# Performance work log

Measured on AMD Instinct MI355X. Metric: run time of the kernel, lower is better.

The kernel has to match this reference:

```python
import jax, jax.numpy as jnp
import numpy as np

INPUT_SIZE = 2048
HIDDEN_SIZE = 2048
BATCH = 8192


def setup_inputs() -> dict:
    key = jax.random.key(0)
    ks = jax.random.split(key, 11)
    comb = INPUT_SIZE + HIDDEN_SIZE
    s = 1.0 / np.sqrt(comb)
    inp = {
        "x": jax.random.normal(ks[0], (BATCH, INPUT_SIZE), jnp.float32),
        "h_prev": jax.random.normal(ks[1], (BATCH, HIDDEN_SIZE), jnp.float32),
        "c_prev": jax.random.normal(ks[2], (BATCH, HIDDEN_SIZE), jnp.float32),
        # torch nn.Linear weights: (out_features, in_features)
        "W_f": jax.random.uniform(ks[3], (HIDDEN_SIZE, comb), jnp.float32, -s, s),
        "b_f": jax.random.uniform(ks[4], (HIDDEN_SIZE,), jnp.float32, -s, s),
        "W_i": jax.random.uniform(ks[5], (HIDDEN_SIZE, comb), jnp.float32, -s, s),
        "b_i": jax.random.uniform(ks[6], (HIDDEN_SIZE,), jnp.float32, -s, s),
        "W_c": jax.random.uniform(ks[7], (HIDDEN_SIZE, comb), jnp.float32, -s, s),
        "b_c": jax.random.uniform(ks[8], (HIDDEN_SIZE,), jnp.float32, -s, s),
        "W_o": jax.random.uniform(ks[9], (HIDDEN_SIZE, comb), jnp.float32, -s, s),
        "b_o": jax.random.uniform(ks[10], (HIDDEN_SIZE,), jnp.float32, -s, s),
    }
    return inp


def reference(x, h_prev, c_prev, W_f, b_f, W_i, b_i, W_c, b_c, W_o, b_o):
    combined = jnp.concatenate([x, h_prev], axis=1)  # [B, in+hid]
    # Fuse the four gate GEMMs into one: stack weights along output dim.
    W_all = jnp.concatenate([W_f, W_i, W_c, W_o], axis=0)  # [4H, in+hid]
    b_all = jnp.concatenate([b_f, b_i, b_c, b_o], axis=0)  # [4H]
    gates = combined @ W_all.T + b_all  # [B, 4H]
    f_lin, i_lin, c_lin, o_lin = jnp.split(gates, 4, axis=1)
    f_t = jax.nn.sigmoid(f_lin)
    i_t = jax.nn.sigmoid(i_lin)
    c_tilde = jnp.tanh(c_lin)
    c_t = f_t * c_prev + i_t * c_tilde
    o_t = jax.nn.sigmoid(o_lin)
    h_t = o_t * jnp.tanh(c_t)
    return (h_t, c_t)
```

## Files before the change

### kernel.cpp

```cpp
#include <hip/hip_runtime.h>
#include <hip/hip_bf16.h>


typedef short bf16x8 __attribute__((ext_vector_type(8)));
typedef float f32x4  __attribute__((ext_vector_type(4)));

#define BATCH 8192
#define INPUT 2048
#define HID   2048
#define KDIM  4096
#define NT_K  64

__device__ __forceinline__ float bf2f(unsigned short u) {
    return __uint_as_float(((unsigned int)u) << 16);
}
__device__ __forceinline__ unsigned short f2bf(float f) {
    unsigned int u = __float_as_uint(f);
    u += 0x7fffu + ((u >> 16) & 1u);
    return (unsigned short)(u >> 16);
}
__device__ __forceinline__ float sigm(float x)  { return 1.0f / (1.0f + __expf(-x)); }
__device__ __forceinline__ float tanh_(float x) { return 2.0f / (1.0f + __expf(-2.0f * x)) - 1.0f; }

__device__ __forceinline__ bool looks_bf16(const unsigned short* p) {
    int lane = threadIdx.x & 63;
    unsigned short v = p[2 * lane];
    int e = (v >> 7) & 0xFF;
    return __all(e >= 90 && e <= 141) != 0;
}

__device__ __forceinline__ bf16x8 sani(bf16x8 v) {
    #pragma unroll
    for (int i = 0; i < 8; ++i) {
        unsigned short u = (unsigned short)v[i];
        if ((u & 0x7F80u) == 0x7F80u) v[i] = 0;
    }
    return v;
}

__device__ __forceinline__ uint2 pack4(float4 v) {
    uint2 r;
    r.x = (unsigned int)f2bf(v.x) | ((unsigned int)f2bf(v.y) << 16);
    r.y = (unsigned int)f2bf(v.z) | ((unsigned int)f2bf(v.w) << 16);
    return r;
}

__device__ __forceinline__ void gload_lds16(const void* g, void* l) {
    __builtin_amdgcn_global_load_lds(
        (const __attribute__((address_space(1))) unsigned int*)g,
        (__attribute__((address_space(3))) unsigned int*)l, 16, 0, 0);
}

#define NCHUNK_SIDE (2048 * 2048)

__global__ __launch_bounds__(256) void pack_ws8(
    const void* __restrict__ x, const void* __restrict__ hprev,
    const void* __restrict__ Wf, const void* __restrict__ Wi,
    const void* __restrict__ Wc, const void* __restrict__ Wo,
    char* __restrict__ Aws, char* __restrict__ Bws)
{
    const bool isb = looks_bf16((const unsigned short*)x);
    const int total = 2 * NCHUNK_SIDE;
    for (int idx = blockIdx.x * 256 + threadIdx.x; idx < total;
         idx += gridDim.x * 256) {
        const int side = (idx >= NCHUNK_SIDE);
        const int c    = side ? idx - NCHUNK_SIDE : idx;
        const int tile = c >> 11;
        const int b16  = c & 2047;
        const int kt   = tile & 63;
        const int tt   = tile >> 6;
        const int half = b16 >> 10;
        const int r_in = (b16 >> 3) & 127;
        const int slot = b16 & 7;
        const int k    = kt * 64 + (slot ^ (r_in & 7)) * 8;

        const void* base;
        size_t soff;
        if (!side) {
            const int R = tt * 256 + half * 128 + r_in;
            if (k < INPUT) { base = x;     soff = (size_t)R * INPUT + k; }
            else           { base = hprev; soff = (size_t)R * HID + (k - INPUT); }
        } else {
            const int P  = half * 128 + r_in;
            const int g  = P >> 6;
            const int wn = (P >> 4) & 3;
            const int cc = P & 15;
            const int h  = tt * 64 + wn * 16 + cc;
            base = (g == 0) ? Wf : (g == 1) ? Wi : (g == 2) ? Wc : Wo;
            soff = (size_t)h * KDIM + k;
        }
        char* dst = (side ? Bws : Aws) + (size_t)c * 16;
        if (isb) {
            bf16x8 v = sani(*(const bf16x8*)((const unsigned short*)base + soff));
            *(bf16x8*)dst = v;
        } else {
            const float* s = (const float*)base + soff;
            float4 v0 = *(const float4*)s;
            float4 v1 = *(const float4*)(s + 4);
            uint2 p0 = pack4(v0), p1 = pack4(v1);
            uint4 o; o.x = p0.x; o.y = p0.y; o.z = p1.x; o.w = p1.y;
            *(uint4*)dst = o;
        }
    }
}

#define VM(n)  asm volatile("s_waitcnt vmcnt(" #n ")" ::: "memory")
#define BAR()  do { asm volatile("" ::: "memory"); \
                    __builtin_amdgcn_s_barrier();  \
                    asm volatile("" ::: "memory"); } while (0)

__global__ __launch_bounds__(512, 2) void lstm_main8(
    const char* __restrict__ Aws, const char* __restrict__ Bws,
    const void* __restrict__ x_orig,
    const void* __restrict__ cprev_v,
    const void* __restrict__ bfp, const void* __restrict__ bip,
    const void* __restrict__ bcp, const void* __restrict__ bop,
    void* __restrict__ out_v)
{
    extern __shared__ __align__(16) char smem[];

    const bool isb = looks_bf16((const unsigned short*)x_orig);

    const int tid   = threadIdx.x;
    const int wid   = tid >> 6;
    const int lane  = tid & 63;
    const int wm    = wid >> 2;
    const int wn    = wid & 3;
    const int lrow  = lane & 15;
    const int chunk = lane >> 4;

    const int bid = blockIdx.x;
    const int swz = (bid & 7) * 128 + (bid >> 3);
    const int mt  = swz >> 5, nt = swz & 31;

    const char* Atile = Aws + (size_t)(mt * 64) * 32768;
    const char* Btile = Bws + (size_t)(nt * 64) * 32768;
    const int stg  = wid * 1024 + lane * 16;
    const int stgl = wid * 1024;

    const int xm = (lrow & 7) << 4;
    int koff[2];
    koff[0] = (chunk * 16) ^ xm;
    koff[1] = (64 + chunk * 16) ^ xm;
    int aoff[8];
    #pragma unroll
    for (int m = 0; m < 8; ++m)
        aoff[m] = (m >> 2) * 16384 + ((((m & 3) * 2 + wm) * 16 + lrow) * 128);
    int boff[4];
    #pragma unroll
    for (int g = 0; g < 4; ++g)
        boff[g] = 32768 + (g >> 1) * 16384 + ((((g & 1) * 4 + wn) * 16 + lrow) * 128);

    const int col_h = nt * 64 + wn * 16 + lrow;
    float bias0, bias1, bias2, bias3;
    if (isb) {
        bias0 = bf2f(((const unsigned short*)bfp)[col_h]);
        bias1 = bf2f(((const unsigned short*)bip)[col_h]);
        bias2 = bf2f(((const unsigned short*)bcp)[col_h]);
        bias3 = bf2f(((const unsigned short*)bop)[col_h]);
    } else {
        bias0 = ((const float*)bfp)[col_h];
        bias1 = ((const float*)bip)[col_h];
        bias2 = ((const float*)bcp)[col_h];
        bias3 = ((const float*)bop)[col_h];
    }

    f32x4 acc[8][4];
    #pragma unroll
    for (int m = 0; m < 8; ++m) {
        acc[m][0] = (f32x4){bias0, bias0, bias0, bias0};
        acc[m][1] = (f32x4){bias1, bias1, bias1, bias1};
        acc[m][2] = (f32x4){bias2, bias2, bias2, bias2};
        acc[m][3] = (f32x4){bias3, bias3, bias3, bias3};
    }

    bf16x8 af[4][2], bf[2][2];

#define STAGE_A(NB, H, T) do { \
        const char* _g = Atile + (size_t)(T) * 32768 + (H) * 16384 + stg; \
        char* _l = smem + (NB) + (H) * 16384 + stgl;                      \
        gload_lds16(_g, _l); gload_lds16(_g + 8192, _l + 8192); } while (0)
#define STAGE_B(NB, H, T) do { \
        const char* _g = Btile + (size_t)(T) * 32768 + (H) * 16384 + stg; \
        char* _l = smem + (NB) + 32768 + (H) * 16384 + stgl;              \
        gload_lds16(_g, _l); gload_lds16(_g + 8192, _l + 8192); } while (0)
#define LOADA(BUFB, MB) do { \
        _Pragma("unroll") for (int mi = 0; mi < 4; ++mi)                  \
        _Pragma("unroll") for (int ks = 0; ks < 2; ++ks)                  \
            af[mi][ks] = *(const bf16x8*)(smem + (BUFB) + aoff[(MB) + mi] + koff[ks]); } while (0)
#define LOADB(BUFB, GB) do { \
        _Pragma("unroll") for (int gi = 0; gi < 2; ++gi)                  \
        _Pragma("unroll") for (int ks = 0; ks < 2; ++ks)                  \
            bf[gi][ks] = *(const bf16x8*)(smem + (BUFB) + boff[(GB) + gi] + koff[ks]); } while (0)
#define MM(MB, GB) do { \
        __builtin_amdgcn_s_setprio(1);                                    \
        _Pragma("unroll") for (int mi = 0; mi < 4; ++mi)                  \
        _Pragma("unroll") for (int gi = 0; gi < 2; ++gi)                  \
        _Pragma("unroll") for (int ks = 0; ks < 2; ++ks)                  \
            acc[(MB) + mi][(GB) + gi] = __builtin_amdgcn_mfma_f32_16x16x32_bf16( \
                af[mi][ks], bf[gi][ks], acc[(MB) + mi][(GB) + gi], 0, 0, 0);      \
        __builtin_amdgcn_s_setprio(0); } while (0)

    STAGE_A(0, 0, 0);
    STAGE_B(0, 0, 0);
    STAGE_B(0, 1, 0);
    STAGE_A(0, 1, 0);

    #pragma unroll 1
    for (int t = 0; t < NT_K - 1; ++t) {
        const int bufb = (t & 1) << 16;
        const int nb   = ((t & 1) ^ 1) << 16;
        STAGE_A(nb, 0, t + 1);
        VM(6); BAR();
        LOADA(bufb, 0); LOADB(bufb, 0);
        MM(0, 0); BAR();
        STAGE_B(nb, 0, t + 1);
        VM(6); BAR();
        LOADB(bufb, 2);
        MM(0, 2); BAR();
        STAGE_B(nb, 1, t + 1);
        VM(6); BAR();
        LOADA(bufb, 4);
        MM(4, 2); BAR();
        STAGE_A(nb, 1, t + 1);
        BAR();
        LOADB(bufb, 0);
        MM(4, 0); BAR();
    }
    {
        const int bufb = ((NT_K - 1) & 1) << 16;
        VM(4); BAR();
        LOADA(bufb, 0); LOADB(bufb, 0);
        MM(0, 0); BAR();
        VM(2); BAR();
        LOADB(bufb, 2);
        MM(0, 2); BAR();
        VM(0); BAR();
        LOADA(bufb, 4);
        MM(4, 2); BAR();
        BAR();
        LOADB(bufb, 0);
        MM(4, 0);
    }

    if (isb) {
        const unsigned short* cp = (const unsigned short*)cprev_v;
        unsigned short* ho = (unsigned short*)out_v;
        unsigned short* co = ho + (size_t)BATCH * HID;
        #pragma unroll
        for (int m = 0; m < 8; ++m) {
            const int row0 = mt * 256 + (m * 2 + wm) * 16 + (lane >> 4) * 4;
            #pragma unroll
            for (int r = 0; r < 4; ++r) {
                const int row = row0 + r;
                float fg = sigm(acc[m][0][r]);
                float ig = sigm(acc[m][1][r]);
                float cg = tanh_(acc[m][2][r]);
                float og = sigm(acc[m][3][r]);
                float cpv = bf2f(cp[(size_t)row * HID + col_h]);
                float ct = fg * cpv + ig * cg;
                float ht = og * tanh_(ct);
                co[(size_t)row * HID + col_h] = f2bf(ct);
                ho[(size_t)row * HID + col_h] = f2bf(ht);
            }
        }
    } else {
        const float* cp = (const float*)cprev_v;
        float* ho = (float*)out_v;
        float* co = ho + (size_t)BATCH * HID;
        #pragma unroll
        for (int m = 0; m < 8; ++m) {
            const int row0 = mt * 256 + (m * 2 + wm) * 16 + (lane >> 4) * 4;
            #pragma unroll
            for (int r = 0; r < 4; ++r) {
                const int row = row0 + r;
                float fg = sigm(acc[m][0][r]);
                float ig = sigm(acc[m][1][r]);
                float cg = tanh_(acc[m][2][r]);
                float og = sigm(acc[m][3][r]);
                float cpv = cp[(size_t)row * HID + col_h];
                float ct = fg * cpv + ig * cg;
                float ht = og * tanh_(ct);
                co[(size_t)row * HID + col_h] = ct;
                ho[(size_t)row * HID + col_h] = ht;
            }
        }
    }
}

__global__ __launch_bounds__(256) void lstm_bf16(
    const unsigned short* __restrict__ x,
    const unsigned short* __restrict__ hprev,
    const unsigned short* __restrict__ cprev,
    const unsigned short* __restrict__ Wf, const unsigned short* __restrict__ bfp,
    const unsigned short* __restrict__ Wi, const unsigned short* __restrict__ bip,
    const unsigned short* __restrict__ Wc, const unsigned short* __restrict__ bcp,
    const unsigned short* __restrict__ Wo, const unsigned short* __restrict__ bop,
    unsigned short* __restrict__ hout, unsigned short* __restrict__ cout)
{
    if (!looks_bf16(x)) return;

    __shared__ __align__(16) unsigned short lds_a[128 * 32];
    __shared__ __align__(16) unsigned short lds_b[128 * 32];

    const int tid  = threadIdx.x;
    const int wave = tid >> 6;
    const int lane = tid & 63;
    const int wm   = wave >> 1;
    const int wn   = wave & 1;
    const int m_base = blockIdx.x * 128;
    const int h_base = blockIdx.y * 32;

    const int rA0 = tid >> 2,        sA = tid & 3;
    const int rA1 = 64 + (tid >> 2);
    const unsigned short* Wsel = (wave == 0) ? Wf : (wave == 1) ? Wi
                               : (wave == 2) ? Wc : Wo;
    const unsigned short* bsrc0 =
        Wsel + (size_t)(h_base + (rA0 & 15)) * KDIM + sA * 8;
    const unsigned short* bsrc1 =
        Wsel + (size_t)(h_base + 16 + (rA1 & 15)) * KDIM + sA * 8;
    const size_t aoff0 = (size_t)(m_base + rA0) * INPUT + sA * 8;
    const size_t aoff1 = (size_t)(m_base + rA1) * INPUT + sA * 8;

    const int lrow = lane & 15, lchunk = lane >> 4;
    const int col_h = h_base + wn * 16 + lrow;

    const float bias0 = bf2f(bfp[col_h]), bias1 = bf2f(bip[col_h]);
    const float bias2 = bf2f(bcp[col_h]), bias3 = bf2f(bop[col_h]);

    f32x4 acc[4][4];
    for (int mi = 0; mi < 4; ++mi) {
        acc[mi][0] = (f32x4){bias0, bias0, bias0, bias0};
        acc[mi][1] = (f32x4){bias1, bias1, bias1, bias1};
        acc[mi][2] = (f32x4){bias2, bias2, bias2, bias2};
        acc[mi][3] = (f32x4){bias3, bias3, bias3, bias3};
    }

    for (int k0 = 0; k0 < KDIM; k0 += 32) {
        const unsigned short* asrc = (k0 < INPUT) ? (x + k0) : (hprev + (k0 - INPUT));
        bf16x8 va0 = sani(*(const bf16x8*)(asrc + aoff0));
        bf16x8 va1 = sani(*(const bf16x8*)(asrc + aoff1));
        bf16x8 vb0 = sani(*(const bf16x8*)(bsrc0 + k0));
        bf16x8 vb1 = sani(*(const bf16x8*)(bsrc1 + k0));

        __syncthreads();
        *(bf16x8*)&lds_a[rA0 * 32 + sA * 8] = va0;
        *(bf16x8*)&lds_a[rA1 * 32 + sA * 8] = va1;
        *(bf16x8*)&lds_b[rA0 * 32 + sA * 8] = vb0;
        *(bf16x8*)&lds_b[rA1 * 32 + sA * 8] = vb1;
        __syncthreads();

        bf16x8 af2[4], bfr[4];
        #pragma unroll
        for (int i = 0; i < 4; ++i) {
            af2[i] = *(const bf16x8*)&lds_a[(wm * 64 + i * 16 + lrow) * 32 + lchunk * 8];
            bfr[i] = *(const bf16x8*)&lds_b[(wn * 64 + i * 16 + lrow) * 32 + lchunk * 8];
        }
        #pragma unroll
        for (int mi = 0; mi < 4; ++mi)
            #pragma unroll
            for (int g = 0; g < 4; ++g)
                acc[mi][g] = __builtin_amdgcn_mfma_f32_16x16x32_bf16(
                                 af2[mi], bfr[g], acc[mi][g], 0, 0, 0);
    }

    #pragma unroll
    for (int mi = 0; mi < 4; ++mi) {
        const int row0 = m_base + wm * 64 + mi * 16 + (lane >> 4) * 4;
        #pragma unroll
        for (int r = 0; r < 4; ++r) {
            const int row = row0 + r;
            float fg = sigm(acc[mi][0][r]);
            float ig = sigm(acc[mi][1][r]);
            float cg = tanh_(acc[mi][2][r]);
            float og = sigm(acc[mi][3][r]);
            float cp = bf2f(cprev[(size_t)row * HID + col_h]);
            float ct = fg * cp + ig * cg;
            float ht = og * tanh_(ct);
            cout[(size_t)row * HID + col_h] = f2bf(ct);
            hout[(size_t)row * HID + col_h] = f2bf(ht);
        }
    }
}

__global__ __launch_bounds__(256) void lstm_f32(
    const float* __restrict__ x,
    const float* __restrict__ hprev,
    const float* __restrict__ cprev,
    const float* __restrict__ Wf, const float* __restrict__ bfp,
    const float* __restrict__ Wi, const float* __restrict__ bip,
    const float* __restrict__ Wc, const float* __restrict__ bcp,
    const float* __restrict__ Wo, const float* __restrict__ bop,
    float* __restrict__ hout, float* __restrict__ cout)
{
    if (looks_bf16((const unsigned short*)x)) return;

    __shared__ __align__(16) unsigned short lds_a[128 * 32];
    __shared__ __align__(16) unsigned short lds_b[128 * 32];

    const int tid  = threadIdx.x;
    const int wave = tid >> 6;
    const int lane = tid & 63;
    const int wm   = wave >> 1;
    const int wn   = wave & 1;
    const int m_base = blockIdx.x * 128;
    const int h_base = blockIdx.y * 32;

    const int s8  = tid >> 3;
    const int sub = tid & 7;
    const float* W4[4] = {Wf, Wi, Wc, Wo};
    size_t aoff2[4];
    const float* bptr[4];
    #pragma unroll
    for (int r = 0; r < 4; ++r) {
        const int row = r * 32 + s8;
        aoff2[r] = (size_t)(m_base + row) * INPUT + sub * 4;
        const int gate = (2 * r + (tid >> 7)) & 3;
        const int wrow = h_base + ((r >> 1) << 4) + (s8 & 15);
        bptr[r] = W4[gate] + (size_t)wrow * KDIM + sub * 4;
    }

    const int lrow = lane & 15, lchunk = lane >> 4;
    const int col_h = h_base + wn * 16 + lrow;

    const float bias0 = bfp[col_h], bias1 = bip[col_h];
    const float bias2 = bcp[col_h], bias3 = bop[col_h];

    f32x4 acc[4][4];
    for (int mi = 0; mi < 4; ++mi) {
        acc[mi][0] = (f32x4){bias0, bias0, bias0, bias0};
        acc[mi][1] = (f32x4){bias1, bias1, bias1, bias1};
        acc[mi][2] = (f32x4){bias2, bias2, bias2, bias2};
        acc[mi][3] = (f32x4){bias3, bias3, bias3, bias3};
    }

    for (int k0 = 0; k0 < KDIM; k0 += 32) {
        const float* asrc = (k0 < INPUT) ? (x + k0) : (hprev + (k0 - INPUT));
        float4 va[4], vb[4];
        #pragma unroll
        for (int r = 0; r < 4; ++r) va[r] = *(const float4*)(asrc + aoff2[r]);
        #pragma unroll
        for (int r = 0; r < 4; ++r) vb[r] = *(const float4*)(bptr[r] + k0);

        __syncthreads();
        #pragma unroll
        for (int r = 0; r < 4; ++r) {
            const int row = r * 32 + s8;
            *(uint2*)&lds_a[row * 32 + sub * 4] = pack4(va[r]);
            *(uint2*)&lds_b[row * 32 + sub * 4] = pack4(vb[r]);
        }
        __syncthreads();

        bf16x8 af2[4], bfr[4];
        #pragma unroll
        for (int i = 0; i < 4; ++i) {
            af2[i] = *(const bf16x8*)&lds_a[(wm * 64 + i * 16 + lrow) * 32 + lchunk * 8];
            bfr[i] = *(const bf16x8*)&lds_b[(wn * 64 + i * 16 + lrow) * 32 + lchunk * 8];
        }
        #pragma unroll
        for (int mi = 0; mi < 4; ++mi)
            #pragma unroll
            for (int g = 0; g < 4; ++g)
                acc[mi][g] = __builtin_amdgcn_mfma_f32_16x16x32_bf16(
                                 af2[mi], bfr[g], acc[mi][g], 0, 0, 0);
    }

    #pragma unroll
    for (int mi = 0; mi < 4; ++mi) {
        const int row0 = m_base + wm * 64 + mi * 16 + (lane >> 4) * 4;
        #pragma unroll
        for (int r = 0; r < 4; ++r) {
            const int row = row0 + r;
            float fg = sigm(acc[mi][0][r]);
            float ig = sigm(acc[mi][1][r]);
            float cg = tanh_(acc[mi][2][r]);
            float og = sigm(acc[mi][3][r]);
            float cp = cprev[(size_t)row * HID + col_h];
            float ct = fg * cp + ig * cg;
            float ht = og * tanh_(ct);
            cout[(size_t)row * HID + col_h] = ct;
            hout[(size_t)row * HID + col_h] = ht;
        }
    }
}

extern "C" void kernel_launch(void* const* d_in, const int* in_sizes, int n_in,
                              void* d_out, int out_size, void* d_ws, size_t ws_size,
                              hipStream_t stream) {
    const size_t WS_NEEDED = (size_t)(BATCH + 4 * HID) * KDIM * sizeof(unsigned short);

    if (ws_size >= WS_NEEDED) {
        char* A_ws = (char*)d_ws;
        char* B_ws = A_ws + (size_t)BATCH * KDIM * 2;

        hipLaunchKernelGGL(pack_ws8, dim3(4096), dim3(256), 0, stream,
                           d_in[0], d_in[1], d_in[3], d_in[5], d_in[7], d_in[9],
                           A_ws, B_ws);

        static int attr_done = 0;
        if (!attr_done) {
            hipFuncSetAttribute(reinterpret_cast<const void*>(lstm_main8),
                                hipFuncAttributeMaxDynamicSharedMemorySize, 131072);
            attr_done = 1;
        }
        hipLaunchKernelGGL(lstm_main8, dim3(1024), dim3(512), 131072, stream,
                           A_ws, B_ws, d_in[0], d_in[2],
                           d_in[4], d_in[6], d_in[8], d_in[10], d_out);
        return;
    }

    dim3 grid(BATCH / 128, HID / 32);
    dim3 block(256);
    {
        const unsigned short* x  = (const unsigned short*)d_in[0];
        const unsigned short* hp = (const unsigned short*)d_in[1];
        const unsigned short* cp = (const unsigned short*)d_in[2];
        unsigned short* hout = (unsigned short*)d_out;
        unsigned short* cout = hout + (size_t)BATCH * HID;
        hipLaunchKernelGGL(lstm_bf16, grid, block, 0, stream, x, hp, cp,
                           (const unsigned short*)d_in[3], (const unsigned short*)d_in[4],
                           (const unsigned short*)d_in[5], (const unsigned short*)d_in[6],
                           (const unsigned short*)d_in[7], (const unsigned short*)d_in[8],
                           (const unsigned short*)d_in[9], (const unsigned short*)d_in[10],
                           hout, cout);
    }
    {
        const float* x  = (const float*)d_in[0];
        const float* hp = (const float*)d_in[1];
        const float* cp = (const float*)d_in[2];
        float* hout = (float*)d_out;
        float* cout = hout + (size_t)BATCH * HID;
        hipLaunchKernelGGL(lstm_f32, grid, block, 0, stream, x, hp, cp,
                           (const float*)d_in[3], (const float*)d_in[4],
                           (const float*)d_in[5], (const float*)d_in[6],
                           (const float*)d_in[7], (const float*)d_in[8],
                           (const float*)d_in[9], (const float*)d_in[10],
                           hout, cout);
    }
}
```

Before: 832.4 us.

## Software-pipeline LDS fragment loads with MFMA and restructure pack kernel

The main GEMM loop now keeps separate register sets for the A row halves and the B gate pairs. This lets each MFMA group run while the next fragments are read from LDS, and the last MFMA of one k-step is deferred into the next iteration. The aim is to hide LDS read latency behind the matrix cores, at the cost of more VGPRs. The pack kernel is also rewritten so each thread handles 8 rows with fixed-stride, nontemporal loads and stores, which removes the grid-stride loop and per-element index math. It now assumes a grid of exactly 2^20 threads.

Measured after the change: 785.7 us. 1.06x faster.

```diff
diff --git a/kernel.cpp b/kernel.cpp
--- a/kernel.cpp
+++ b/kernel.cpp
@@ -4,6 +4,7 @@
 
 typedef short bf16x8 __attribute__((ext_vector_type(8)));
 typedef float f32x4  __attribute__((ext_vector_type(4)));
+typedef unsigned int u32x4 __attribute__((ext_vector_type(4)));
 
 #define BATCH 8192
 #define INPUT 2048
@@ -38,10 +39,10 @@
     return v;
 }
 
-__device__ __forceinline__ uint2 pack4(float4 v) {
+__device__ __forceinline__ uint2 pack4v(f32x4 v) {
     uint2 r;
-    r.x = (unsigned int)f2bf(v.x) | ((unsigned int)f2bf(v.y) << 16);
-    r.y = (unsigned int)f2bf(v.z) | ((unsigned int)f2bf(v.w) << 16);
+    r.x = (unsigned int)f2bf(v[0]) | ((unsigned int)f2bf(v[1]) << 16);
+    r.y = (unsigned int)f2bf(v[2]) | ((unsigned int)f2bf(v[3]) << 16);
     return r;
 }
 
@@ -50,8 +51,6 @@
         (const __attribute__((address_space(1))) unsigned int*)g,
         (__attribute__((address_space(3))) unsigned int*)l, 16, 0, 0);
 }
-
-#define NCHUNK_SIDE (2048 * 2048)
 
 __global__ __launch_bounds__(256) void pack_ws8(
     const void* __restrict__ x, const void* __restrict__ hprev,
@@ -60,46 +59,51 @@
     char* __restrict__ Aws, char* __restrict__ Bws)
 {
     const bool isb = looks_bf16((const unsigned short*)x);
-    const int total = 2 * NCHUNK_SIDE;
-    for (int idx = blockIdx.x * 256 + threadIdx.x; idx < total;
-         idx += gridDim.x * 256) {
-        const int side = (idx >= NCHUNK_SIDE);
-        const int c    = side ? idx - NCHUNK_SIDE : idx;
-        const int tile = c >> 11;
-        const int b16  = c & 2047;
-        const int kt   = tile & 63;
-        const int tt   = tile >> 6;
-        const int half = b16 >> 10;
-        const int r_in = (b16 >> 3) & 127;
-        const int slot = b16 & 7;
-        const int k    = kt * 64 + (slot ^ (r_in & 7)) * 8;
-
-        const void* base;
-        size_t soff;
-        if (!side) {
-            const int R = tt * 256 + half * 128 + r_in;
-            if (k < INPUT) { base = x;     soff = (size_t)R * INPUT + k; }
-            else           { base = hprev; soff = (size_t)R * HID + (k - INPUT); }
-        } else {
-            const int P  = half * 128 + r_in;
-            const int g  = P >> 6;
-            const int wn = (P >> 4) & 3;
-            const int cc = P & 15;
-            const int h  = tt * 64 + wn * 16 + cc;
-            base = (g == 0) ? Wf : (g == 1) ? Wi : (g == 2) ? Wc : Wo;
-            soff = (size_t)h * KDIM + k;
-        }
-        char* dst = (side ? Bws : Aws) + (size_t)c * 16;
-        if (isb) {
-            bf16x8 v = sani(*(const bf16x8*)((const unsigned short*)base + soff));
-            *(bf16x8*)dst = v;
-        } else {
-            const float* s = (const float*)base + soff;
-            float4 v0 = *(const float4*)s;
-            float4 v1 = *(const float4*)(s + 4);
-            uint2 p0 = pack4(v0), p1 = pack4(v1);
-            uint4 o; o.x = p0.x; o.y = p0.y; o.z = p1.x; o.w = p1.y;
-            *(uint4*)dst = o;
+    const unsigned int u = blockIdx.x * 256 + threadIdx.x;
+    const int slot = u & 7;
+    const int rgrp = (u >> 3) & 15;
+    const int half = (u >> 7) & 1;
+    const int tile = (u >> 8) & 2047;
+    const int side = u >> 19;
+    const int kt = tile & 63, tt = tile >> 6;
+
+    const void* base;
+    size_t src0;
+    int stride;
+    if (!side) {
+        const int row0 = tt * 256 + half * 128 + rgrp * 8;
+        if (kt < 32) { base = x;     src0 = (size_t)row0 * INPUT + kt * 64; }
+        else         { base = hprev; src0 = (size_t)row0 * HID + (kt - 32) * 64; }
+        stride = INPUT;
+    } else {
+        const int P0 = half * 128 + rgrp * 8;
+        const int g = P0 >> 6, wn = (P0 >> 4) & 3, cc0 = P0 & 15;
+        const int h0 = tt * 64 + wn * 16 + cc0;
+        base = (g == 0) ? Wf : (g == 1) ? Wi : (g == 2) ? Wc : Wo;
+        src0 = (size_t)h0 * KDIM + kt * 64;
+        stride = KDIM;
+    }
+    char* dst0 = (side ? Bws : Aws) +
+                 ((size_t)tile * 32768 + half * 16384 + rgrp * 1024 + slot * 16);
+
+    if (isb) {
+        const unsigned short* s0 = (const unsigned short*)base + src0;
+        #pragma unroll
+        for (int i = 0; i < 8; ++i) {
+            bf16x8 v = sani(__builtin_nontemporal_load(
+                (const bf16x8*)(s0 + (size_t)i * stride + ((slot ^ i) << 3))));
+            __builtin_nontemporal_store(v, (bf16x8*)(dst0 + i * 128));
+        }
+    } else {
+        const float* s0 = (const float*)base + src0;
+        #pragma unroll
+        for (int i = 0; i < 8; ++i) {
+            const float* s = s0 + (size_t)i * stride + ((slot ^ i) << 3);
+            f32x4 v0 = __builtin_nontemporal_load((const f32x4*)s);
+            f32x4 v1 = __builtin_nontemporal_load((const f32x4*)(s + 4));
+            uint2 p0 = pack4v(v0), p1 = pack4v(v1);
+            u32x4 o = (u32x4){p0.x, p0.y, p1.x, p1.y};
+            __builtin_nontemporal_store(o, (u32x4*)(dst0 + i * 128));
         }
     }
 }
@@ -174,7 +178,7 @@
         acc[m][3] = (f32x4){bias3, bias3, bias3, bias3};
     }
 
-    bf16x8 af[4][2], bf[2][2];
+    bf16x8 af03[4][2], af47[4][2], b01[2][2], b23[2][2];
 
 #define STAGE_A(NB, H, T) do { \
         const char* _g = Atile + (size_t)(T) * 32768 + (H) * 16384 + stg; \
@@ -184,21 +188,21 @@
         const char* _g = Btile + (size_t)(T) * 32768 + (H) * 16384 + stg; \
         char* _l = smem + (NB) + 32768 + (H) * 16384 + stgl;              \
         gload_lds16(_g, _l); gload_lds16(_g + 8192, _l + 8192); } while (0)
-#define LOADA(BUFB, MB) do { \
+#define LDA(DST, BUFB, MB) do { \
         _Pragma("unroll") for (int mi = 0; mi < 4; ++mi)                  \
         _Pragma("unroll") for (int ks = 0; ks < 2; ++ks)                  \
-            af[mi][ks] = *(const bf16x8*)(smem + (BUFB) + aoff[(MB) + mi] + koff[ks]); } while (0)
-#define LOADB(BUFB, GB) do { \
+            DST[mi][ks] = *(const bf16x8*)(smem + (BUFB) + aoff[(MB) + mi] + koff[ks]); } while (0)
+#define LDB(DST, BUFB, GB) do { \
         _Pragma("unroll") for (int gi = 0; gi < 2; ++gi)                  \
         _Pragma("unroll") for (int ks = 0; ks < 2; ++ks)                  \
-            bf[gi][ks] = *(const bf16x8*)(smem + (BUFB) + boff[(GB) + gi] + koff[ks]); } while (0)
-#define MM(MB, GB) do { \
+            DST[gi][ks] = *(const bf16x8*)(smem + (BUFB) + boff[(GB) + gi] + koff[ks]); } while (0)
+#define MM(AF, BF, MB, GB) do { \
         __builtin_amdgcn_s_setprio(1);                                    \
         _Pragma("unroll") for (int mi = 0; mi < 4; ++mi)                  \
         _Pragma("unroll") for (int gi = 0; gi < 2; ++gi)                  \
         _Pragma("unroll") for (int ks = 0; ks < 2; ++ks)                  \
             acc[(MB) + mi][(GB) + gi] = __builtin_amdgcn_mfma_f32_16x16x32_bf16( \
-                af[mi][ks], bf[gi][ks], acc[(MB) + mi][(GB) + gi], 0, 0, 0);      \
+                AF[mi][ks], BF[gi][ks], acc[(MB) + mi][(GB) + gi], 0, 0, 0);      \
         __builtin_amdgcn_s_setprio(0); } while (0)
 
     STAGE_A(0, 0, 0);
@@ -208,39 +212,43 @@
 
     #pragma unroll 1
     for (int t = 0; t < NT_K - 1; ++t) {
-        const int bufb = (t & 1) << 16;
-        const int nb   = ((t & 1) ^ 1) << 16;
+        const int cb = (t & 1) << 16;
+        const int nb = cb ^ (1 << 16);
         STAGE_A(nb, 0, t + 1);
         VM(6); BAR();
-        LOADA(bufb, 0); LOADB(bufb, 0);
-        MM(0, 0); BAR();
+        if (t) MM(af47, b01, 4, 0);
+        LDA(af03, cb, 0); LDB(b01, cb, 0);
+        BAR();
         STAGE_B(nb, 0, t + 1);
         VM(6); BAR();
-        LOADB(bufb, 2);
-        MM(0, 2); BAR();
+        MM(af03, b01, 0, 0);
+        LDB(b23, cb, 2);
+        BAR();
         STAGE_B(nb, 1, t + 1);
         VM(6); BAR();
-        LOADA(bufb, 4);
-        MM(4, 2); BAR();
+        MM(af03, b23, 0, 2);
+        LDA(af47, cb, 4);
+        BAR();
         STAGE_A(nb, 1, t + 1);
         BAR();
-        LOADB(bufb, 0);
-        MM(4, 0); BAR();
+        MM(af47, b23, 4, 2);
+        BAR();
     }
     {
-        const int bufb = ((NT_K - 1) & 1) << 16;
+        const int cb = ((NT_K - 1) & 1) << 16;
         VM(4); BAR();
-        LOADA(bufb, 0); LOADB(bufb, 0);
-        MM(0, 0); BAR();
+        MM(af47, b01, 4, 0);
+        LDA(af03, cb, 0); LDB(b01, cb, 0);
+        BAR();
         VM(2); BAR();
-        LOADB(bufb, 2);
-        MM(0, 2); BAR();
+        MM(af03, b01, 0, 0);
+        LDB(b23, cb, 2);
+        BAR();
         VM(0); BAR();
-        LOADA(bufb, 4);
-        MM(4, 2); BAR();
-        BAR();
-        LOADB(bufb, 0);
-        MM(4, 0);
+        MM(af03, b23, 0, 2);
+        LDA(af47, cb, 4);
+        MM(af47, b23, 4, 2);
+        MM(af47, b01, 4, 0);
     }
 
     if (isb) {
@@ -446,8 +454,14 @@
         #pragma unroll
         for (int r = 0; r < 4; ++r) {
             const int row = r * 32 + s8;
-            *(uint2*)&lds_a[row * 32 + sub * 4] = pack4(va[r]);
-            *(uint2*)&lds_b[row * 32 + sub * 4] = pack4(vb[r]);
+            float4 a = va[r], b = vb[r];
+            uint2 pa, pb;
+            pa.x = (unsigned int)f2bf(a.x) | ((unsigned int)f2bf(a.y) << 16);
+            pa.y = (unsigned int)f2bf(a.z) | ((unsigned int)f2bf(a.w) << 16);
+            pb.x = (unsigned int)f2bf(b.x) | ((unsigned int)f2bf(b.y) << 16);
+            pb.y = (unsigned int)f2bf(b.z) | ((unsigned int)f2bf(b.w) << 16);
+            *(uint2*)&lds_a[row * 32 + sub * 4] = pa;
+            *(uint2*)&lds_b[row * 32 + sub * 4] = pb;
         }
         __syncthreads();
 
```
